# Performance work log

Hardware: AMD Instinct MI355X
Metric: run time of the kernel (lower is better)

## Reference

```python
import jax, jax.numpy as jnp
import numpy as np

B, D, C = 2048, 512, 50000
MARGIN = 0.3
SCALE = 30.0
EPS = 1e-12


def setup_inputs() -> dict:
    key = jax.random.key(0)
    k1, k2, k3 = jax.random.split(key, 3)
    embeddings = jax.random.normal(k1, (B, D), dtype=jnp.float32)
    labels = jax.random.randint(k2, (B,), 0, C, dtype=jnp.int64)
    # Xavier-uniform init for weight (num_classes, in_features)
    limit = float(np.sqrt(6.0 / (C + D)))
    weight = jax.random.uniform(k3, (C, D), dtype=jnp.float32, minval=-limit, maxval=limit)
    return {"embeddings": embeddings, "labels": labels, "weight": weight}


def _l2_normalize(x, axis):
    # Matches torch F.normalize(p=2, eps=1e-12): x / max(||x||, eps)
    norm = jnp.sqrt(jnp.sum(x * x, axis=axis, keepdims=True))
    return x / jnp.maximum(norm, EPS)


def reference(embeddings, labels, weight):
    emb_n = _l2_normalize(embeddings, axis=1)            # (B, D)
    w_n = _l2_normalize(weight, axis=1)                  # (C, D)
    cos = jnp.einsum("bd,cd->bc", emb_n, w_n)            # (B, C)
    # margin subtract at label index (avoid dense one-hot materialization)
    rows = jnp.arange(cos.shape[0])
    phi = cos.at[rows, labels].add(-MARGIN)
    logits = phi * SCALE
    # cross-entropy with mean reduction
    logp = jax.nn.log_softmax(logits, axis=-1)
    nll = -jnp.take_along_axis(logp, labels[:, None], axis=-1)[:, 0]
    return jnp.mean(nll)
```

## Files before the change

### kernel.cpp

```cpp
#include <hip/hip_runtime.h>
#include <hip/hip_bf16.h>
#include <math.h>
#include <stdint.h>


#define B_ROWS    2048
#define D_DIM     512
#define C_CLASSES 50000
#define C_PAD     50048
#define NCHUNK    391
#define CPX       49
#define ARC_MARGIN 0.3f
#define ARC_SCALE  30.0f
#define ARC_EPS    1e-12f
#define K_LOG2E_S  43.2808512f

#define OFF_WQ    0u
#define OFF_EMBQ  25624576u
#define OFF_WINV  26673152u
#define OFF_EINV  26873152u
#define OFF_PART  26881344u

typedef __attribute__((ext_vector_type(8))) int   i32x8;
typedef __attribute__((ext_vector_type(4))) int   i32x4;
typedef __attribute__((ext_vector_type(4))) float f32x4;

typedef __attribute__((address_space(1))) const unsigned int g_u32;
typedef __attribute__((address_space(3))) unsigned int       l_u32;

__device__ __forceinline__ void gload_lds16(const void* g, void* l) {
    g_u32* gp = (g_u32*)(uintptr_t)g;
    l_u32* lp = (l_u32*)(uintptr_t)l;
    __builtin_amdgcn_global_load_lds(gp, lp, 16, 0, 0);
}

__global__ __launch_bounds__(256) void k_prep(const float* __restrict__ emb,
                                              const float* __restrict__ weight,
                                              uint8_t* __restrict__ embq,
                                              uint8_t* __restrict__ wq,
                                              float* __restrict__ einv,
                                              float* __restrict__ winv,
                                              float* __restrict__ out) {
    if (blockIdx.x == 0 && threadIdx.x == 0) out[0] = 0.f;
    int wave = blockIdx.x * (blockDim.x >> 6) + (threadIdx.x >> 6);
    int lane = threadIdx.x & 63;
    int g0   = wave << 2;

    const float* src;
    uint8_t* dst;
    float* invout;
    if (g0 >= C_PAD) {
        int row = g0 - C_PAD;
        src = emb + (size_t)row * D_DIM;
        dst = embq + (size_t)row * D_DIM;
        invout = einv + row;
    } else if (g0 >= C_CLASSES) {
        int2 z = make_int2(0, 0);
        #pragma unroll
        for (int r = 0; r < 4; ++r)
            *(int2*)(wq + (size_t)(g0 + r) * D_DIM + lane * 8) = z;
        return;
    } else {
        src = weight + (size_t)g0 * D_DIM;
        dst = wq + (size_t)g0 * D_DIM;
        invout = winv + g0;
    }

    const float4* r4 = (const float4*)src;
    float4 v[8];
    #pragma unroll
    for (int r = 0; r < 4; ++r) {
        v[2 * r]     = r4[r * 128 + lane * 2];
        v[2 * r + 1] = r4[r * 128 + lane * 2 + 1];
    }

    #pragma unroll
    for (int r = 0; r < 4; ++r) {
        float4 v0 = v[2 * r], v1 = v[2 * r + 1];
        float s = v0.x*v0.x + v0.y*v0.y + v0.z*v0.z + v0.w*v0.w
                + v1.x*v1.x + v1.y*v1.y + v1.z*v1.z + v1.w*v1.w;
        #pragma unroll
        for (int off = 32; off; off >>= 1) s += __shfl_xor(s, off);
        float rn = 1.0f / fmaxf(sqrtf(s), ARC_EPS);
        if (lane == 0) invout[r] = rn;
        int p0 = __builtin_amdgcn_cvt_pk_fp8_f32(v0.x * rn, v0.y * rn, 0, false);
        p0     = __builtin_amdgcn_cvt_pk_fp8_f32(v0.z * rn, v0.w * rn, p0, true);
        int p1 = __builtin_amdgcn_cvt_pk_fp8_f32(v1.x * rn, v1.y * rn, 0, false);
        p1     = __builtin_amdgcn_cvt_pk_fp8_f32(v1.z * rn, v1.w * rn, p1, true);
        *(int2*)(dst + (size_t)r * D_DIM + lane * 8) = make_int2(p0, p1);
    }
}

struct TrueT  { static constexpr bool value = true;  };
struct FalseT { static constexpr bool value = false; };

__global__ __launch_bounds__(256) void k_gemm(const uint8_t* __restrict__ embq,
                                              const uint8_t* __restrict__ wq,
                                              float* __restrict__ partials) {
    __shared__ __align__(16) uint8_t A_s[128 * 128];
    __shared__ __align__(16) uint8_t B_s[128 * 128];
    __shared__ float Red[128][2];

    const int tid    = threadIdx.x;
    const int w      = tid >> 6;
    const int lane   = tid & 63;
    const int lanelo = lane & 15;
    const int quad   = lane >> 4;
    const int wrow0  = (w >> 1) * 64;
    const int wcol0  = (w & 1) * 64;

    const int id    = blockIdx.x;
    const int xcd   = id & 7;
    const int s     = id >> 3;
    const int rb_   = s & 15;
    const int chunk = xcd * CPX + (s >> 4);
    if (chunk >= NCHUNK) return;
    const int b0 = rb_ * 128;
    const int n0 = chunk * 128;

    const uint8_t* Abase = embq + (size_t)b0 * D_DIM;
    const uint8_t* Bbase = wq   + (size_t)n0 * D_DIM;

    f32x4 acc[4][4];
    #pragma unroll
    for (int i = 0; i < 4; ++i)
        #pragma unroll
        for (int j = 0; j < 4; ++j)
            acc[i][j] = (f32x4){0.f, 0.f, 0.f, 0.f};

    const int srow = lane & 15;
    const int skc  = lane >> 4;

    auto stage = [&](int kt) {
        const int k0 = kt * 128;
        #pragma unroll
        for (int t = 0; t < 2; ++t) {
            const int rb = w * 2 + t;
            #pragma unroll
            for (int h = 0; h < 2; ++h) {
                const int kc = h * 4 + skc;
                gload_lds16(Abase + (size_t)(rb * 16 + srow) * D_DIM + k0 + kc * 16,
                            &A_s[rb * 2048 + h * 1024]);
                gload_lds16(Bbase + (size_t)(rb * 16 + srow) * D_DIM + k0 + kc * 16,
                            &B_s[rb * 2048 + h * 1024]);
            }
        }
    };

    stage(0);
    #pragma unroll
    for (int kt = 0; kt < 4; ++kt) {
        __syncthreads();

        i32x8 af[4], bfr[4];
        #pragma unroll
        for (int i = 0; i < 4; ++i) {
            const int rb = (w >> 1) * 4 + i;
            i32x4 lo = *(const i32x4*)&A_s[rb * 2048 + quad * 512 + lanelo * 16];
            i32x4 hi = *(const i32x4*)&A_s[rb * 2048 + quad * 512 + 256 + lanelo * 16];
            af[i] = (i32x8){lo[0], lo[1], lo[2], lo[3], hi[0], hi[1], hi[2], hi[3]};
        }
        #pragma unroll
        for (int j = 0; j < 4; ++j) {
            const int rb = (w & 1) * 4 + j;
            i32x4 lo = *(const i32x4*)&B_s[rb * 2048 + quad * 512 + lanelo * 16];
            i32x4 hi = *(const i32x4*)&B_s[rb * 2048 + quad * 512 + 256 + lanelo * 16];
            bfr[j] = (i32x8){lo[0], lo[1], lo[2], lo[3], hi[0], hi[1], hi[2], hi[3]};
        }
        __syncthreads();

        if (kt < 3) stage(kt + 1);

        #pragma unroll
        for (int i = 0; i < 4; ++i)
            #pragma unroll
            for (int j = 0; j < 4; ++j)
                acc[i][j] = __builtin_amdgcn_mfma_scale_f32_16x16x128_f8f6f4(
                    af[i], bfr[j], acc[i][j],
                    0, 0,
                    0, 127,
                    0, 127);
    }

    auto epi = [&](auto maskTag) {
        constexpr bool MASK = decltype(maskTag)::value;
        #pragma unroll
        for (int i = 0; i < 4; ++i) {
            #pragma unroll
            for (int reg = 0; reg < 4; ++reg) {
                float s4 = 0.f;
                #pragma unroll
                for (int j = 0; j < 4; ++j) {
                    float t = __builtin_amdgcn_exp2f(
                        fmaf(acc[i][j][reg], K_LOG2E_S, -K_LOG2E_S));
                    if (MASK) {
                        int c = n0 + wcol0 + j * 16 + lanelo;
                        if (c >= C_CLASSES) t = 0.f;
                    }
                    s4 += t;
                }
                #pragma unroll
                for (int off = 1; off < 16; off <<= 1)
                    s4 += __shfl_xor(s4, off);
                if (lanelo == 0)
                    Red[wrow0 + i * 16 + quad * 4 + reg][w & 1] = s4;
            }
        }
    };
    if (chunk == NCHUNK - 1) epi(TrueT{}); else epi(FalseT{});
    __syncthreads();

    if (tid < 128)
        partials[(size_t)(b0 + tid) * NCHUNK + chunk] = Red[tid][0] + Red[tid][1];
}

__global__ __launch_bounds__(256) void k_fin(const float* __restrict__ emb,
                                             const float* __restrict__ weight,
                                             const float* __restrict__ einv,
                                             const float* __restrict__ winv,
                                             const int* __restrict__ labels,
                                             const float* __restrict__ partials,
                                             float* __restrict__ out) {
    __shared__ float s_dot[2], s_ls[2];
    int widx = threadIdx.x >> 6;
    int lane = threadIdx.x & 63;
    int rloc = widx & 1;
    int role = widx >> 1;
    int b    = blockIdx.x * 2 + rloc;

    if (role == 0) {
        int label = labels[b];
        const float4* e  = (const float4*)(emb + (size_t)b * D_DIM);
        const float4* wt = (const float4*)(weight + (size_t)label * D_DIM);
        float4 e0 = e[lane],  e1 = e[lane + 64];
        float4 w0 = wt[lane], w1 = wt[lane + 64];
        float dot = e0.x*w0.x + e0.y*w0.y + e0.z*w0.z + e0.w*w0.w
                  + e1.x*w1.x + e1.y*w1.y + e1.z*w1.z + e1.w*w1.w;
        #pragma unroll
        for (int off = 32; off; off >>= 1) dot += __shfl_xor(dot, off);
        if (lane == 0) s_dot[rloc] = dot;
    } else {
        float p[7];
        #pragma unroll
        for (int t = 0; t < 7; ++t) {
            int idx = lane + t * 64;
            p[t] = (idx < NCHUNK) ? partials[(size_t)b * NCHUNK + idx] : 0.f;
        }
        float ls = p[0];
        #pragma unroll
        for (int t = 1; t < 7; ++t) ls += p[t];
        #pragma unroll
        for (int off = 32; off; off >>= 1) ls += __shfl_xor(ls, off);
        if (lane == 0) s_ls[rloc] = ls;
    }
    __syncthreads();

    if (threadIdx.x < 2) {
        int r = threadIdx.x;
        int b2 = blockIdx.x * 2 + r;
        int label = labels[b2];
        float cosv   = s_dot[r] * einv[b2] * winv[label];
        float l_orig = ARC_SCALE * cosv;
        float l_adj  = ARC_SCALE * (cosv - ARC_MARGIN);
        float s_adj = s_ls[r] - __expf(l_orig - ARC_SCALE) + __expf(l_adj - ARC_SCALE);
        float v = ARC_SCALE + logf(s_adj) - l_adj;
        atomicAdd(out, v * (1.0f / (float)B_ROWS));
    }
}

extern "C" void kernel_launch(void* const* d_in, const int* in_sizes, int n_in,
                              void* d_out, int out_size, void* d_ws, size_t ws_size,
                              hipStream_t stream) {
    const float* emb    = (const float*)d_in[0];
    const int*   labels = (const int*)d_in[1];
    const float* weight = (const float*)d_in[2];
    float* out = (float*)d_out;

    char* ws = (char*)d_ws;
    uint8_t* wq    = (uint8_t*)(ws + OFF_WQ);
    uint8_t* embq  = (uint8_t*)(ws + OFF_EMBQ);
    float* winv     = (float*)(ws + OFF_WINV);
    float* einv     = (float*)(ws + OFF_EINV);
    float* partials = (float*)(ws + OFF_PART);

    k_prep<<<(C_PAD + B_ROWS) / 16, 256, 0, stream>>>(emb, weight, embq, wq,
                                                      einv, winv, out);

    k_gemm<<<8 * CPX * 16, 256, 0, stream>>>(embq, wq, partials);

    k_fin<<<B_ROWS / 2, 256, 0, stream>>>(emb, weight, einv, winv, labels,
                                          partials, out);
}
```

Before: 276.3 us.

## Enlarge GEMM tile to 256x256 with double-buffered LDS and 512 threads

The fused cosine-GEMM/exp-sum kernel now computes 256x256 output tiles with 8 waves per block instead of 128x128 with 4 waves. It adds double-buffered LDS staging so the next K slice loads while the current one feeds MFMA, which removes one barrier per iteration. The chunk-to-XCD mapping becomes interleaved, and the partials array shrinks to 196 chunks per row. Each wave now holds 32 accumulators, which raises register pressure. The tile uses 128KB of shared memory, so occupancy may be limited.

```diff
diff --git a/kernel.cpp b/kernel.cpp
--- a/kernel.cpp
+++ b/kernel.cpp
@@ -7,19 +7,18 @@
 #define B_ROWS    2048
 #define D_DIM     512
 #define C_CLASSES 50000
-#define C_PAD     50048
-#define NCHUNK    391
-#define CPX       49
+#define C_PAD     50176
+#define NCHUNK    196
 #define ARC_MARGIN 0.3f
 #define ARC_SCALE  30.0f
 #define ARC_EPS    1e-12f
 #define K_LOG2E_S  43.2808512f
 
 #define OFF_WQ    0u
-#define OFF_EMBQ  25624576u
-#define OFF_WINV  26673152u
-#define OFF_EINV  26873152u
-#define OFF_PART  26881344u
+#define OFF_EMBQ  25690112u
+#define OFF_WINV  26738688u
+#define OFF_EINV  26938688u
+#define OFF_PART  26946880u
 
 typedef __attribute__((ext_vector_type(8))) int   i32x8;
 typedef __attribute__((ext_vector_type(4))) int   i32x4;
@@ -94,92 +93,94 @@
 struct TrueT  { static constexpr bool value = true;  };
 struct FalseT { static constexpr bool value = false; };
 
-__global__ __launch_bounds__(256) void k_gemm(const uint8_t* __restrict__ embq,
-                                              const uint8_t* __restrict__ wq,
-                                              float* __restrict__ partials) {
-    __shared__ __align__(16) uint8_t A_s[128 * 128];
-    __shared__ __align__(16) uint8_t B_s[128 * 128];
-    __shared__ float Red[128][2];
+__global__ __launch_bounds__(512, 2) void k_gemm(const uint8_t* __restrict__ embq,
+                                                 const uint8_t* __restrict__ wq,
+                                                 float* __restrict__ partials) {
+    __shared__ __align__(16) uint8_t SMEM[2][65536];
+    float (*Red)[2] = (float (*)[2])&SMEM[0][0];
 
     const int tid    = threadIdx.x;
     const int w      = tid >> 6;
     const int lane   = tid & 63;
     const int lanelo = lane & 15;
     const int quad   = lane >> 4;
-    const int wrow0  = (w >> 1) * 64;
-    const int wcol0  = (w & 1) * 64;
+    const int wr     = w >> 1;
+    const int wc     = w & 1;
 
     const int id    = blockIdx.x;
     const int xcd   = id & 7;
-    const int s     = id >> 3;
-    const int rb_   = s & 15;
-    const int chunk = xcd * CPX + (s >> 4);
+    const int slot  = id >> 3;
+    const int rb_   = slot & 7;
+    const int ci    = slot >> 3;
+    const int chunk = xcd + (ci << 3);
     if (chunk >= NCHUNK) return;
-    const int b0 = rb_ * 128;
-    const int n0 = chunk * 128;
+    const int b0 = rb_ * 256;
+    const int n0 = chunk * 256;
 
     const uint8_t* Abase = embq + (size_t)b0 * D_DIM;
     const uint8_t* Bbase = wq   + (size_t)n0 * D_DIM;
 
-    f32x4 acc[4][4];
+    f32x4 acc[4][8];
     #pragma unroll
     for (int i = 0; i < 4; ++i)
         #pragma unroll
-        for (int j = 0; j < 4; ++j)
+        for (int j = 0; j < 8; ++j)
             acc[i][j] = (f32x4){0.f, 0.f, 0.f, 0.f};
 
     const int srow = lane & 15;
     const int skc  = lane >> 4;
 
-    auto stage = [&](int kt) {
+    auto stage = [&](int bufsel, int kt) {
+        uint8_t* dstA = &SMEM[bufsel][0];
+        uint8_t* dstB = &SMEM[bufsel][32768];
         const int k0 = kt * 128;
         #pragma unroll
         for (int t = 0; t < 2; ++t) {
             const int rb = w * 2 + t;
+            const size_t go = (size_t)(rb * 16 + srow) * D_DIM + k0;
             #pragma unroll
             for (int h = 0; h < 2; ++h) {
                 const int kc = h * 4 + skc;
-                gload_lds16(Abase + (size_t)(rb * 16 + srow) * D_DIM + k0 + kc * 16,
-                            &A_s[rb * 2048 + h * 1024]);
-                gload_lds16(Bbase + (size_t)(rb * 16 + srow) * D_DIM + k0 + kc * 16,
-                            &B_s[rb * 2048 + h * 1024]);
+                gload_lds16(Abase + go + kc * 16, dstA + rb * 2048 + h * 1024);
+                gload_lds16(Bbase + go + kc * 16, dstB + rb * 2048 + h * 1024);
             }
         }
     };
 
-    stage(0);
+    stage(0, 0);
+    __syncthreads();
+
     #pragma unroll
     for (int kt = 0; kt < 4; ++kt) {
-        __syncthreads();
-
-        i32x8 af[4], bfr[4];
+        const int buf = kt & 1;
+        if (kt < 3) stage(buf ^ 1, kt + 1);
+
+        const uint8_t* Abuf = &SMEM[buf][0];
+        const uint8_t* Bbuf = &SMEM[buf][32768];
+
+        i32x8 af[4];
         #pragma unroll
         for (int i = 0; i < 4; ++i) {
-            const int rb = (w >> 1) * 4 + i;
-            i32x4 lo = *(const i32x4*)&A_s[rb * 2048 + quad * 512 + lanelo * 16];
-            i32x4 hi = *(const i32x4*)&A_s[rb * 2048 + quad * 512 + 256 + lanelo * 16];
+            const int rb = wr * 4 + i;
+            i32x4 lo = *(const i32x4*)&Abuf[rb * 2048 + quad * 512 + lanelo * 16];
+            i32x4 hi = *(const i32x4*)&Abuf[rb * 2048 + quad * 512 + 256 + lanelo * 16];
             af[i] = (i32x8){lo[0], lo[1], lo[2], lo[3], hi[0], hi[1], hi[2], hi[3]};
         }
         #pragma unroll
-        for (int j = 0; j < 4; ++j) {
-            const int rb = (w & 1) * 4 + j;
-            i32x4 lo = *(const i32x4*)&B_s[rb * 2048 + quad * 512 + lanelo * 16];
-            i32x4 hi = *(const i32x4*)&B_s[rb * 2048 + quad * 512 + 256 + lanelo * 16];
-            bfr[j] = (i32x8){lo[0], lo[1], lo[2], lo[3], hi[0], hi[1], hi[2], hi[3]};
-        }
-        __syncthreads();
-
-        if (kt < 3) stage(kt + 1);
-
-        #pragma unroll
-        for (int i = 0; i < 4; ++i)
+        for (int j = 0; j < 8; ++j) {
+            const int rb = wc * 8 + j;
+            i32x4 lo = *(const i32x4*)&Bbuf[rb * 2048 + quad * 512 + lanelo * 16];
+            i32x4 hi = *(const i32x4*)&Bbuf[rb * 2048 + quad * 512 + 256 + lanelo * 16];
+            i32x8 bf = (i32x8){lo[0], lo[1], lo[2], lo[3], hi[0], hi[1], hi[2], hi[3]};
             #pragma unroll
-            for (int j = 0; j < 4; ++j)
+            for (int i = 0; i < 4; ++i)
                 acc[i][j] = __builtin_amdgcn_mfma_scale_f32_16x16x128_f8f6f4(
-                    af[i], bfr[j], acc[i][j],
+                    af[i], bf, acc[i][j],
                     0, 0,
                     0, 127,
                     0, 127);
+        }
+        __syncthreads();
     }
 
     auto epi = [&](auto maskTag) {
@@ -190,11 +191,11 @@
             for (int reg = 0; reg < 4; ++reg) {
                 float s4 = 0.f;
                 #pragma unroll
-                for (int j = 0; j < 4; ++j) {
+                for (int j = 0; j < 8; ++j) {
                     float t = __builtin_amdgcn_exp2f(
                         fmaf(acc[i][j][reg], K_LOG2E_S, -K_LOG2E_S));
                     if (MASK) {
-                        int c = n0 + wcol0 + j * 16 + lanelo;
+                        int c = n0 + wc * 128 + j * 16 + lanelo;
                         if (c >= C_CLASSES) t = 0.f;
                     }
                     s4 += t;
@@ -203,14 +204,14 @@
                 for (int off = 1; off < 16; off <<= 1)
                     s4 += __shfl_xor(s4, off);
                 if (lanelo == 0)
-                    Red[wrow0 + i * 16 + quad * 4 + reg][w & 1] = s4;
+                    Red[wr * 64 + i * 16 + quad * 4 + reg][wc] = s4;
             }
         }
     };
     if (chunk == NCHUNK - 1) epi(TrueT{}); else epi(FalseT{});
     __syncthreads();
 
-    if (tid < 128)
+    if (tid < 256)
         partials[(size_t)(b0 + tid) * NCHUNK + chunk] = Red[tid][0] + Red[tid][1];
 }
 
@@ -240,15 +241,15 @@
         for (int off = 32; off; off >>= 1) dot += __shfl_xor(dot, off);
         if (lane == 0) s_dot[rloc] = dot;
     } else {
-        float p[7];
-        #pragma unroll
-        for (int t = 0; t < 7; ++t) {
+        float p[4];
+        #pragma unroll
+        for (int t = 0; t < 4; ++t) {
             int idx = lane + t * 64;
             p[t] = (idx < NCHUNK) ? partials[(size_t)b * NCHUNK + idx] : 0.f;
         }
         float ls = p[0];
         #pragma unroll
-        for (int t = 1; t < 7; ++t) ls += p[t];
+        for (int t = 1; t < 4; ++t) ls += p[t];
         #pragma unroll
         for (int off = 32; off; off >>= 1) ls += __shfl_xor(ls, off);
         if (lane == 0) s_ls[rloc] = ls;
@@ -286,7 +287,7 @@
     k_prep<<<(C_PAD + B_ROWS) / 16, 256, 0, stream>>>(emb, weight, embq, wq,
                                                       einv, winv, out);
 
-    k_gemm<<<8 * CPX * 16, 256, 0, stream>>>(embq, wq, partials);
+    k_gemm<<<1600, 512, 0, stream>>>(embq, wq, partials);
 
     k_fin<<<B_ROWS / 2, 256, 0, stream>>>(emb, weight, einv, winv, labels,
                                           partials, out);
```

After: 440.8 us. +59.5%, slower.
